# Optimization experiments

Hardware: AMD Instinct MI355X
Metric: run time of the kernel (lower is better)

## Reference

```python
import jax, jax.numpy as jnp
import numpy as np

B, H, E_DIM, V = 512, 2048, 1024, 50257


def setup_inputs() -> dict:
    key = jax.random.key(0)
    ks = jax.random.split(key, 10)
    s_e = 1.0 / np.sqrt(E_DIM)
    s_h = 1.0 / np.sqrt(H)
    return {
        "inp": jax.random.randint(ks[0], (B,), 0, V),
        "h_0": jax.random.normal(ks[1], (B, H), jnp.float32) * 0.1,
        "c_0": jax.random.normal(ks[2], (B, H), jnp.float32) * 0.1,
        "E": jax.random.normal(ks[3], (V, E_DIM), jnp.float32),
        "Wx": jax.random.normal(ks[4], (4, H, E_DIM), jnp.float32) * s_e,
        "bx": jax.random.normal(ks[5], (4, H), jnp.float32) * s_e,
        "Wh": jax.random.normal(ks[6], (4, H, H), jnp.float32) * s_h,
        "bh": jax.random.normal(ks[7], (4, H), jnp.float32) * s_h,
        "Wd": jax.random.normal(ks[8], (V, H), jnp.float32) * s_h,
        "bd": jax.random.normal(ks[9], (V,), jnp.float32) * s_h,
    }


def reference(inp, h_0, c_0, E, Wx, bx, Wh, bh, Wd, bd):
    # Embedding lookup: [B, E_DIM]
    x = E[inp]
    # Two fused GEMMs for all 4 gates (gate order: f, i, o, c): [B, 4, H]
    gates = (jnp.einsum('be,ghe->bgh', x, Wx) + bx[None]
             + jnp.einsum('bh,gkh->bgk', h_0, Wh) + bh[None])
    f_g = jax.nn.sigmoid(gates[:, 0])
    i_g = jax.nn.sigmoid(gates[:, 1])
    o_g = jax.nn.sigmoid(gates[:, 2])
    c_tilda = jnp.tanh(gates[:, 3])
    cx = f_g * c_0 + i_g * c_tilda
    hx = o_g * jnp.tanh(cx)
    out = hx @ Wd.T + bd  # [B, V]
    return out, hx, cx
```

## Files before the change

kernel.cpp:

```cpp
#include <hip/hip_runtime.h>
#include <hip/hip_bf16.h>

using bf16x8 = __attribute__((ext_vector_type(8))) short;
using f32x4  = __attribute__((ext_vector_type(4))) float;

#define DEVI __device__ __forceinline__

DEVI unsigned short bf16r(float f)
{
    return __builtin_bit_cast(unsigned short, __float2bfloat16(f));
}

DEVI bf16x8 cvt8(const f32x4 a, const f32x4 b)
{
    bf16x8 r;
#pragma unroll
    for (int j = 0; j < 4; ++j) {
        r[j]     = (short)bf16r(a[j]);
        r[4 + j] = (short)bf16r(b[j]);
    }
    return r;
}

__global__ __launch_bounds__(256) void k_gather(const float* __restrict__ E,
                                                const int* __restrict__ inp,
                                                unsigned short* __restrict__ x)
{
    const int b = blockIdx.x;
    const long r = inp[b];
    const f32x4 v = ((const f32x4*)(E + r * 1024L))[threadIdx.x];
    ushort4 o;
    o.x = bf16r(v[0]); o.y = bf16r(v[1]); o.z = bf16r(v[2]); o.w = bf16r(v[3]);
    ((ushort4*)(x + (long)b * 1024L))[threadIdx.x] = o;
}

__global__ __launch_bounds__(256) void k_cvt(const float* __restrict__ in,
                                             unsigned short* __restrict__ out)
{
    const long i = (blockIdx.x * 256L + threadIdx.x) * 8;
    const f32x4 a = *(const f32x4*)(in + i);
    const f32x4 b = *(const f32x4*)(in + i + 4);
    *(bf16x8*)(out + i) = cvt8(a, b);
}


DEVI bf16x8 lds_frag(const char* lds, int row, int j)
{
    return *(const bf16x8*)(lds + row * 128 + ((j ^ (row & 7)) << 4));
}

DEVI void mfma_tile(const char* sA, const char* sB, int l, int wr, int wc,
                    f32x4 (&acc)[4][4])
{
#pragma unroll
    for (int ks = 0; ks < 2; ++ks) {
        bf16x8 af[4], bq[4];
#pragma unroll
        for (int m = 0; m < 4; ++m)
            af[m] = lds_frag(sA, wr * 64 + m * 16 + (l & 15), ks * 4 + (l >> 4));
#pragma unroll
        for (int n = 0; n < 4; ++n)
            bq[n] = lds_frag(sB, wc * 64 + n * 16 + (l & 15), ks * 4 + (l >> 4));
#pragma unroll
        for (int m = 0; m < 4; ++m)
#pragma unroll
            for (int n = 0; n < 4; ++n)
                acc[m][n] = __builtin_amdgcn_mfma_f32_16x16x32_bf16(
                    af[m], bq[n], acc[m][n], 0, 0, 0);
    }
}

template <bool CLAMP>
DEVI void gemm_core(const unsigned short* __restrict__ A, long lda, long arow0,
                    const float* __restrict__ B, long ldb, long brow0, long bmax,
                    int ntiles, long kbase, int t,
                    char* sA0, char* sB0, char* sA1, char* sB1,
                    f32x4 (&acc)[4][4])
{
    const int l = t & 63;
    const int wr = (t >> 7) & 1, wc = (t >> 6) & 1;

    const unsigned short* ap[4];
#pragma unroll
    for (int i = 0; i < 4; ++i) {
        const int g = i * 256 + t, row = g >> 3, js = g & 7;
        ap[i] = A + (arow0 + row) * lda + kbase + (long)((js ^ (row & 7)) * 8);
    }
    const float* bp[4];
    int swz[4];
#pragma unroll
    for (int i = 0; i < 4; ++i) {
        const int g = i * 256 + t, row = g >> 3, j = g & 7;
        long br = brow0 + row;
        if (CLAMP) br = (br < bmax) ? br : (bmax - 1);
        bp[i] = B + br * ldb + kbase + (long)(j * 8);
        swz[i] = row * 128 + ((j ^ (row & 7)) << 4);
    }

    f32x4 b0lo[4], b0hi[4], b1lo[4], b1hi[4];

#define LOADB(lo, hi)                                                          \
    do {                                                                       \
        _Pragma("unroll") for (int i = 0; i < 4; ++i) {                        \
            lo[i] = *(const f32x4*)bp[i];                                      \
            hi[i] = *(const f32x4*)(bp[i] + 4);                                \
            bp[i] += 64;                                                       \
        }                                                                      \
    } while (0)
#define DMA_A(buf)                                                             \
    do {                                                                       \
        _Pragma("unroll") for (int i = 0; i < 4; ++i) {                        \
            __builtin_amdgcn_global_load_lds(                                  \
                (const __attribute__((address_space(1))) void*)(ap[i]),        \
                (__attribute__((address_space(3))) void*)((buf) +              \
                                                          (i * 256 + t) * 16), \
                16, 0, 0);                                                     \
            ap[i] += 64;                                                       \
        }                                                                      \
    } while (0)
#define WRITEB(buf, lo, hi)                                                    \
    do {                                                                       \
        _Pragma("unroll") for (int i = 0; i < 4; ++i)                          \
            *(bf16x8*)((buf) + swz[i]) = cvt8(lo[i], hi[i]);                   \
    } while (0)

    LOADB(b0lo, b0hi);
    DMA_A(sA0);
    WRITEB(sB0, b0lo, b0hi);
    LOADB(b1lo, b1hi);
    __syncthreads();

    for (int ti = 0; ti < ntiles; ti += 2) {
        DMA_A(sA1);
        if (ti + 2 < ntiles) LOADB(b0lo, b0hi);
        WRITEB(sB1, b1lo, b1hi);
        mfma_tile(sA0, sB0, l, wr, wc, acc);
        __syncthreads();
        if (ti + 2 < ntiles) {
            DMA_A(sA0);
            if (ti + 3 < ntiles) LOADB(b1lo, b1hi);
            WRITEB(sB0, b0lo, b0hi);
        }
        mfma_tile(sA1, sB1, l, wr, wc, acc);
        __syncthreads();
    }
#undef LOADB
#undef DMA_A
#undef WRITEB
}

__global__ __launch_bounds__(256, 2) void k_gates(
    const unsigned short* __restrict__ xb, const float* __restrict__ Wx,
    const unsigned short* __restrict__ h0b, const float* __restrict__ Wh,
    float* __restrict__ g0, float* __restrict__ g1, float* __restrict__ g2)
{
    __shared__ __align__(16) char sA0[128 * 128], sB0[128 * 128];
    __shared__ __align__(16) char sA1[128 * 128], sB1[128 * 128];
    const int t = threadIdx.x;
    const int bid = blockIdx.x;
    const int xcd = bid & 7, slot = bid >> 3;
    const int L = xcd * 96 + slot;
    const int mtile = L & 3;
    const int rest = L >> 2;
    const int ntile = rest & 63;
    const int z = rest >> 6;

    const unsigned short* A; const float* B; long lda, ldb, kbase; float* C;
    if (z == 0)      { A = xb;  lda = 1024; B = Wx; ldb = 1024; kbase = 0;    C = g0; }
    else if (z == 1) { A = h0b; lda = 2048; B = Wh; ldb = 2048; kbase = 0;    C = g1; }
    else             { A = h0b; lda = 2048; B = Wh; ldb = 2048; kbase = 1024; C = g2; }

    f32x4 acc[4][4] = {};
    gemm_core<false>(A, lda, (long)mtile * 128, B, ldb, (long)ntile * 128,
                     1L << 40, 16, kbase, t, sA0, sB0, sA1, sB1, acc);

    const int l = t & 63;
    const int wr = (t >> 7) & 1, wc = (t >> 6) & 1;
    const int lc = l & 15, r4 = (l >> 4) * 4;
#pragma unroll
    for (int n = 0; n < 4; ++n) {
        const long col = (long)ntile * 128 + wc * 64 + n * 16 + lc;
#pragma unroll
        for (int m = 0; m < 4; ++m) {
            const long row = (long)mtile * 128 + wr * 64 + m * 16 + r4;
#pragma unroll
            for (int r = 0; r < 4; ++r)
                C[(row + r) * 8192 + col] = acc[m][n][r];
        }
    }
}

__global__ __launch_bounds__(256, 2) void k_dec(
    const unsigned short* __restrict__ hxb, const float* __restrict__ Wd,
    const float* __restrict__ bd, float* __restrict__ out)
{
    __shared__ __align__(16) char sA0[128 * 128], sB0[128 * 128];
    __shared__ __align__(16) char sA1[128 * 128], sB1[128 * 128];
    const int t = threadIdx.x;
    const int bid = blockIdx.x;
    const int xcd = bid & 7, slot = bid >> 3;
    const int L = xcd * 196 + (xcd < 4 ? xcd : 4) + slot;
    const int mtile = L & 3;
    const int ntile = L >> 2;
    const long N = 50257;

    f32x4 acc[4][4] = {};
    gemm_core<true>(hxb, 2048, (long)mtile * 128, Wd, 2048, (long)ntile * 128,
                    N, 32, 0, t, sA0, sB0, sA1, sB1, acc);

    const int l = t & 63;
    const int wr = (t >> 7) & 1, wc = (t >> 6) & 1;
    const int lc = l & 15, r4 = (l >> 4) * 4;
#pragma unroll
    for (int n = 0; n < 4; ++n) {
        const long col = (long)ntile * 128 + wc * 64 + n * 16 + lc;
        if (col >= N) continue;
        const float bias = bd[col];
#pragma unroll
        for (int m = 0; m < 4; ++m) {
            const long row = (long)mtile * 128 + wr * 64 + m * 16 + r4;
#pragma unroll
            for (int r = 0; r < 4; ++r)
                out[(row + r) * N + col] = acc[m][n][r] + bias;
        }
    }
}

__global__ __launch_bounds__(256) void k_lstm(
    const float* __restrict__ g0, const float* __restrict__ g1,
    const float* __restrict__ g2, const float* __restrict__ bx,
    const float* __restrict__ bh, const float* __restrict__ c0,
    float* __restrict__ hx, float* __restrict__ cx,
    unsigned short* __restrict__ hxb)
{
    const int i = blockIdx.x * 256 + threadIdx.x;
    const int b = i >> 9;
    const int hc = (i & 511) << 2;
    const long base = (long)b * 8192;

    f32x4 g[4];
#pragma unroll
    for (int gi = 0; gi < 4; ++gi) {
        const long off = base + gi * 2048 + hc;
        const int boff = gi * 2048 + hc;
        g[gi] = *(const f32x4*)(g0 + off);
        g[gi] += *(const f32x4*)(g1 + off);
        g[gi] += *(const f32x4*)(g2 + off);
        g[gi] += *(const f32x4*)(bx + boff);
        g[gi] += *(const f32x4*)(bh + boff);
    }
    const f32x4 c0v = *(const f32x4*)(c0 + (long)b * 2048 + hc);

    f32x4 cv, hv;
    ushort4 hb;
#pragma unroll
    for (int j = 0; j < 4; ++j) {
        const float fg = 1.f / (1.f + __expf(-g[0][j]));
        const float ig = 1.f / (1.f + __expf(-g[1][j]));
        const float og = 1.f / (1.f + __expf(-g[2][j]));
        const float e2 = __expf(2.f * g[3][j]);
        const float ct = 1.f - 2.f / (e2 + 1.f);
        const float c  = fg * c0v[j] + ig * ct;
        const float e2c = __expf(2.f * c);
        const float th  = 1.f - 2.f / (e2c + 1.f);
        cv[j] = c;
        hv[j] = og * th;
    }
    hb.x = bf16r(hv[0]); hb.y = bf16r(hv[1]); hb.z = bf16r(hv[2]); hb.w = bf16r(hv[3]);

    const long o = (long)b * 2048 + hc;
    *(f32x4*)(cx + o) = cv;
    *(f32x4*)(hx + o) = hv;
    *(ushort4*)(hxb + o) = hb;
}

extern "C" void kernel_launch(void* const* d_in, const int* in_sizes, int n_in,
                              void* d_out, int out_size, void* d_ws, size_t ws_size,
                              hipStream_t stream)
{
    const int*   inp = (const int*)d_in[0];
    const float* h0  = (const float*)d_in[1];
    const float* c0  = (const float*)d_in[2];
    const float* E   = (const float*)d_in[3];
    const float* Wx  = (const float*)d_in[4];
    const float* bx  = (const float*)d_in[5];
    const float* Wh  = (const float*)d_in[6];
    const float* bh  = (const float*)d_in[7];
    const float* Wd  = (const float*)d_in[8];
    const float* bd  = (const float*)d_in[9];

    float* out = (float*)d_out;
    float* hx  = out + 512L * 50257L;
    float* cx  = hx + 512L * 2048L;

    unsigned short* xb  = (unsigned short*)out;
    float* g0 = out + (1L << 20);
    float* g1 = out + (5L << 20);
    float* g2 = out + (9L << 20);
    unsigned short* h0b = (unsigned short*)(out + (13L << 20));
    unsigned short* hxb = (unsigned short*)d_ws;

    k_gather<<<512, 256, 0, stream>>>(E, inp, xb);
    k_cvt<<<512, 256, 0, stream>>>(h0, h0b);

    k_gates<<<768, 256, 0, stream>>>(xb, Wx, h0b, Wh, g0, g1, g2);

    k_lstm<<<1024, 256, 0, stream>>>(g0, g1, g2, bx, bh, c0, hx, cx, hxb);

    k_dec<<<1572, 256, 0, stream>>>(hxb, Wd, bd, out);
}
```

Measured before the change: 285.6 us.

## Triple-buffer A tiles and replace syncthreads with fine-grained vmcnt waits

The GEMM core pipeline is restructured to use three LDS buffers for the DMA'd A tiles and two for B, with explicit s_waitcnt vmcnt/lgkmcnt and raw s_barrier in place of __syncthreads. This lets the next A tile's global-to-LDS load be issued before the current tile's MFMAs without a full drain of outstanding memory ops, aiming to overlap loads with compute more deeply. LDS use per block rises from 64KB to 80KB, which may reduce occupancy at two blocks per CU. The hand-tuned vmcnt counts depend on the exact number of outstanding loads and are fragile if the load pattern changes.

```diff
diff --git a/kernel.cpp b/kernel.cpp
--- a/kernel.cpp
+++ b/kernel.cpp
@@ -74,7 +74,7 @@
 DEVI void gemm_core(const unsigned short* __restrict__ A, long lda, long arow0,
                     const float* __restrict__ B, long ldb, long brow0, long bmax,
                     int ntiles, long kbase, int t,
-                    char* sA0, char* sB0, char* sA1, char* sB1,
+                    char* sA , char* sB ,
                     f32x4 (&acc)[4][4])
 {
     const int l = t & 63;
@@ -107,46 +107,64 @@
             bp[i] += 64;                                                       \
         }                                                                      \
     } while (0)
-#define DMA_A(buf)                                                             \
+#define DMA_A(bufidx)                                                          \
     do {                                                                       \
+        char* _d = sA + (bufidx) * 16384;                                      \
         _Pragma("unroll") for (int i = 0; i < 4; ++i) {                        \
             __builtin_amdgcn_global_load_lds(                                  \
                 (const __attribute__((address_space(1))) void*)(ap[i]),        \
-                (__attribute__((address_space(3))) void*)((buf) +              \
+                (__attribute__((address_space(3))) void*)(_d +                 \
                                                           (i * 256 + t) * 16), \
                 16, 0, 0);                                                     \
             ap[i] += 64;                                                       \
         }                                                                      \
     } while (0)
-#define WRITEB(buf, lo, hi)                                                    \
+#define WRITEB(bufofs, lo, hi)                                                 \
     do {                                                                       \
         _Pragma("unroll") for (int i = 0; i < 4; ++i)                          \
-            *(bf16x8*)((buf) + swz[i]) = cvt8(lo[i], hi[i]);                   \
+            *(bf16x8*)(sB + (bufofs) + swz[i]) = cvt8(lo[i], hi[i]);           \
     } while (0)
+#define WAITV12 asm volatile("s_waitcnt vmcnt(12)" ::: "memory")
+#define WAITV0  asm volatile("s_waitcnt vmcnt(0)" ::: "memory")
+#define WAITL0  asm volatile("s_waitcnt lgkmcnt(0)" ::: "memory")
+#define BARRIER __builtin_amdgcn_s_barrier()
 
     LOADB(b0lo, b0hi);
-    DMA_A(sA0);
-    WRITEB(sB0, b0lo, b0hi);
+    DMA_A(0);
+
+    int abuf = 0;
+    for (int ti = 0; ti < ntiles - 2; ti += 2) {
+        LOADB(b1lo, b1hi);
+        DMA_A((abuf + 1) % 3);
+        WAITV12;
+        WRITEB(0, b0lo, b0hi);
+        WAITL0; BARRIER;
+        mfma_tile(sA + abuf * 16384, sB, l, wr, wc, acc);
+        LOADB(b0lo, b0hi);
+        DMA_A((abuf + 2) % 3);
+        WAITV12;
+        WRITEB(16384, b1lo, b1hi);
+        WAITL0; BARRIER;
+        mfma_tile(sA + ((abuf + 1) % 3) * 16384, sB + 16384, l, wr, wc, acc);
+        abuf = (abuf + 2) % 3;
+    }
     LOADB(b1lo, b1hi);
-    __syncthreads();
-
-    for (int ti = 0; ti < ntiles; ti += 2) {
-        DMA_A(sA1);
-        if (ti + 2 < ntiles) LOADB(b0lo, b0hi);
-        WRITEB(sB1, b1lo, b1hi);
-        mfma_tile(sA0, sB0, l, wr, wc, acc);
-        __syncthreads();
-        if (ti + 2 < ntiles) {
-            DMA_A(sA0);
-            if (ti + 3 < ntiles) LOADB(b1lo, b1hi);
-            WRITEB(sB0, b0lo, b0hi);
-        }
-        mfma_tile(sA1, sB1, l, wr, wc, acc);
-        __syncthreads();
-    }
+    DMA_A((abuf + 1) % 3);
+    WAITV12;
+    WRITEB(0, b0lo, b0hi);
+    WAITL0; BARRIER;
+    mfma_tile(sA + abuf * 16384, sB, l, wr, wc, acc);
+    WAITV0;
+    WRITEB(16384, b1lo, b1hi);
+    WAITL0; BARRIER;
+    mfma_tile(sA + ((abuf + 1) % 3) * 16384, sB + 16384, l, wr, wc, acc);
 #undef LOADB
 #undef DMA_A
 #undef WRITEB
+#undef WAITV12
+#undef WAITV0
+#undef WAITL0
+#undef BARRIER
 }
 
 __global__ __launch_bounds__(256, 2) void k_gates(
@@ -154,8 +172,8 @@
     const unsigned short* __restrict__ h0b, const float* __restrict__ Wh,
     float* __restrict__ g0, float* __restrict__ g1, float* __restrict__ g2)
 {
-    __shared__ __align__(16) char sA0[128 * 128], sB0[128 * 128];
-    __shared__ __align__(16) char sA1[128 * 128], sB1[128 * 128];
+    __shared__ __align__(16) char sA[3 * 16384];
+    __shared__ __align__(16) char sB[2 * 16384];
     const int t = threadIdx.x;
     const int bid = blockIdx.x;
     const int xcd = bid & 7, slot = bid >> 3;
@@ -172,7 +190,7 @@
 
     f32x4 acc[4][4] = {};
     gemm_core<false>(A, lda, (long)mtile * 128, B, ldb, (long)ntile * 128,
-                     1L << 40, 16, kbase, t, sA0, sB0, sA1, sB1, acc);
+                     1L << 40, 16, kbase, t, sA, sB, acc);
 
     const int l = t & 63;
     const int wr = (t >> 7) & 1, wc = (t >> 6) & 1;
@@ -194,8 +212,8 @@
     const unsigned short* __restrict__ hxb, const float* __restrict__ Wd,
     const float* __restrict__ bd, float* __restrict__ out)
 {
-    __shared__ __align__(16) char sA0[128 * 128], sB0[128 * 128];
-    __shared__ __align__(16) char sA1[128 * 128], sB1[128 * 128];
+    __shared__ __align__(16) char sA[3 * 16384];
+    __shared__ __align__(16) char sB[2 * 16384];
     const int t = threadIdx.x;
     const int bid = blockIdx.x;
     const int xcd = bid & 7, slot = bid >> 3;
@@ -206,7 +224,7 @@
 
     f32x4 acc[4][4] = {};
     gemm_core<true>(hxb, 2048, (long)mtile * 128, Wd, 2048, (long)ntile * 128,
-                    N, 32, 0, t, sA0, sB0, sA1, sB1, acc);
+                    N, 32, 0, t, sA, sB, acc);
 
     const int l = t & 63;
     const int wr = (t >> 7) & 1, wc = (t >> 6) & 1;
```

New measurement: 305.1 us. 6.8% more time.

## Use 256x128 tiles with 8 waves and register-staged A loads

Applied to the files above, without the earlier changes.

Grows the GEMM block tile from 128x128 to 256x128 and runs 8 waves (512 threads) per block, so each fp32 weight tile converted to bf16 is reused across twice as many batch rows. Weight traffic and conversion work for the large decoder GEMM should roughly halve. A is now loaded through registers and written to LDS instead of the direct global-to-LDS path, with hand-placed vmcnt/lgkmcnt waits and raw barriers. The kernels also need 96KB of dynamic LDS, which may limit how many blocks fit per CU, and the manual waitcnt scheduling is fragile.

```diff
diff --git a/kernel.cpp b/kernel.cpp
--- a/kernel.cpp
+++ b/kernel.cpp
@@ -34,8 +34,8 @@
     ((ushort4*)(x + (long)b * 1024L))[threadIdx.x] = o;
 }
 
-__global__ __launch_bounds__(256) void k_cvt(const float* __restrict__ in,
-                                             unsigned short* __restrict__ out)
+__global__ __launch_bounds__(256) void k_cvtn(const float* __restrict__ in,
+                                              unsigned short* __restrict__ out)
 {
     const long i = (blockIdx.x * 256L + threadIdx.x) * 8;
     const f32x4 a = *(const f32x4*)(in + i);
@@ -49,8 +49,8 @@
     return *(const bf16x8*)(lds + row * 128 + ((j ^ (row & 7)) << 4));
 }
 
-DEVI void mfma_tile(const char* sA, const char* sB, int l, int wr, int wc,
-                    f32x4 (&acc)[4][4])
+DEVI void mfma_tile8(const char* sA, const char* sB, int l, int wr, int wc,
+                     f32x4 (&acc)[4][4])
 {
 #pragma unroll
     for (int ks = 0; ks < 2; ++ks) {
@@ -71,118 +71,122 @@
 }
 
 template <bool CLAMP>
-DEVI void gemm_core(const unsigned short* __restrict__ A, long lda, long arow0,
-                    const float* __restrict__ B, long ldb, long brow0, long bmax,
-                    int ntiles, long kbase, int t,
-                    char* sA0, char* sB0, char* sA1, char* sB1,
-                    f32x4 (&acc)[4][4])
-{
-    const int l = t & 63;
-    const int wr = (t >> 7) & 1, wc = (t >> 6) & 1;
+DEVI void gemm_core8(const unsigned short* __restrict__ A, long lda, long arow0,
+                     const float* __restrict__ B, long ldb, long brow0, long bmax,
+                     int nt, long kbase, int t, char* lds, f32x4 (&acc)[4][4])
+{
+    char* sA0 = lds;
+    char* sA1 = lds + 32768;
+    char* sB0 = lds + 65536;
+    char* sB1 = lds + 81920;
+    const int l = t & 63, w = t >> 6, wr = w >> 1, wc = w & 1;
 
     const unsigned short* ap[4];
+    int aswz[4];
 #pragma unroll
     for (int i = 0; i < 4; ++i) {
-        const int g = i * 256 + t, row = g >> 3, js = g & 7;
-        ap[i] = A + (arow0 + row) * lda + kbase + (long)((js ^ (row & 7)) * 8);
-    }
-    const float* bp[4];
-    int swz[4];
-#pragma unroll
-    for (int i = 0; i < 4; ++i) {
-        const int g = i * 256 + t, row = g >> 3, j = g & 7;
+        const int g = i * 512 + t, row = g >> 3, j = g & 7;
+        ap[i] = A + (arow0 + row) * lda + kbase + j * 8;
+        aswz[i] = row * 128 + ((j ^ (row & 7)) << 4);
+    }
+    const float* bp[2];
+    int bswz[2];
+#pragma unroll
+    for (int i = 0; i < 2; ++i) {
+        const int g = i * 512 + t, row = g >> 3, j = g & 7;
         long br = brow0 + row;
         if (CLAMP) br = (br < bmax) ? br : (bmax - 1);
-        bp[i] = B + br * ldb + kbase + (long)(j * 8);
-        swz[i] = row * 128 + ((j ^ (row & 7)) << 4);
-    }
-
-    f32x4 b0lo[4], b0hi[4], b1lo[4], b1hi[4];
-
-#define LOADB(lo, hi)                                                          \
+        bp[i] = B + br * ldb + kbase + j * 8;
+        bswz[i] = row * 128 + ((j ^ (row & 7)) << 4);
+    }
+
+    bf16x8 ra0[4], ra1[4];
+    f32x4 rb0[4], rb1[4];
+
+#define LOADR(as, bs)                                                          \
     do {                                                                       \
         _Pragma("unroll") for (int i = 0; i < 4; ++i) {                        \
-            lo[i] = *(const f32x4*)bp[i];                                      \
-            hi[i] = *(const f32x4*)(bp[i] + 4);                                \
+            as[i] = *(const bf16x8*)ap[i];                                     \
+            ap[i] += 64;                                                       \
+        }                                                                      \
+        _Pragma("unroll") for (int i = 0; i < 2; ++i) {                        \
+            bs[2 * i]     = *(const f32x4*)bp[i];                              \
+            bs[2 * i + 1] = *(const f32x4*)(bp[i] + 4);                        \
             bp[i] += 64;                                                       \
         }                                                                      \
     } while (0)
-#define DMA_A(buf)                                                             \
-    do {                                                                       \
-        _Pragma("unroll") for (int i = 0; i < 4; ++i) {                        \
-            __builtin_amdgcn_global_load_lds(                                  \
-                (const __attribute__((address_space(1))) void*)(ap[i]),        \
-                (__attribute__((address_space(3))) void*)((buf) +              \
-                                                          (i * 256 + t) * 16), \
-                16, 0, 0);                                                     \
-            ap[i] += 64;                                                       \
-        }                                                                      \
-    } while (0)
-#define WRITEB(buf, lo, hi)                                                    \
+#define WRLDS(sa, sb, as, bs)                                                  \
     do {                                                                       \
         _Pragma("unroll") for (int i = 0; i < 4; ++i)                          \
-            *(bf16x8*)((buf) + swz[i]) = cvt8(lo[i], hi[i]);                   \
+            *(bf16x8*)((sa) + aswz[i]) = as[i];                                \
+        _Pragma("unroll") for (int i = 0; i < 2; ++i)                          \
+            *(bf16x8*)((sb) + bswz[i]) = cvt8(bs[2 * i], bs[2 * i + 1]);       \
     } while (0)
-
-    LOADB(b0lo, b0hi);
-    DMA_A(sA0);
-    WRITEB(sB0, b0lo, b0hi);
-    LOADB(b1lo, b1hi);
-    __syncthreads();
-
-    for (int ti = 0; ti < ntiles; ti += 2) {
-        DMA_A(sA1);
-        if (ti + 2 < ntiles) LOADB(b0lo, b0hi);
-        WRITEB(sB1, b1lo, b1hi);
-        mfma_tile(sA0, sB0, l, wr, wc, acc);
-        __syncthreads();
-        if (ti + 2 < ntiles) {
-            DMA_A(sA0);
-            if (ti + 3 < ntiles) LOADB(b1lo, b1hi);
-            WRITEB(sB0, b0lo, b0hi);
+#define WAITV8  asm volatile("s_waitcnt vmcnt(8)" ::: "memory")
+#define WAITV0  asm volatile("s_waitcnt vmcnt(0)" ::: "memory")
+#define WAITL0  asm volatile("s_waitcnt lgkmcnt(0)" ::: "memory")
+#define BARRIER __builtin_amdgcn_s_barrier()
+
+    LOADR(ra0, rb0);
+    LOADR(ra1, rb1);
+    WAITV8;
+    WRLDS(sA0, sB0, ra0, rb0);
+    LOADR(ra0, rb0);
+    WAITL0; BARRIER;
+
+    for (int kt = 0; kt < nt; kt += 2) {
+        if (kt + 2 < nt) WAITV8; else WAITV0;
+        WRLDS(sA1, sB1, ra1, rb1);
+        if (kt + 3 < nt) LOADR(ra1, rb1);
+        mfma_tile8(sA0, sB0, l, wr, wc, acc);
+        WAITL0; BARRIER;
+        if (kt + 2 < nt) {
+            if (kt + 3 < nt) WAITV8; else WAITV0;
+            WRLDS(sA0, sB0, ra0, rb0);
+            if (kt + 4 < nt) LOADR(ra0, rb0);
         }
-        mfma_tile(sA1, sB1, l, wr, wc, acc);
-        __syncthreads();
-    }
-#undef LOADB
-#undef DMA_A
-#undef WRITEB
-}
-
-__global__ __launch_bounds__(256, 2) void k_gates(
+        mfma_tile8(sA1, sB1, l, wr, wc, acc);
+        WAITL0; BARRIER;
+    }
+#undef LOADR
+#undef WRLDS
+#undef WAITV8
+#undef WAITV0
+#undef WAITL0
+#undef BARRIER
+}
+
+__global__ __launch_bounds__(512, 2) void k_gates(
     const unsigned short* __restrict__ xb, const float* __restrict__ Wx,
     const unsigned short* __restrict__ h0b, const float* __restrict__ Wh,
     float* __restrict__ g0, float* __restrict__ g1, float* __restrict__ g2)
 {
-    __shared__ __align__(16) char sA0[128 * 128], sB0[128 * 128];
-    __shared__ __align__(16) char sA1[128 * 128], sB1[128 * 128];
+    extern __shared__ __align__(16) char lds[];
     const int t = threadIdx.x;
     const int bid = blockIdx.x;
     const int xcd = bid & 7, slot = bid >> 3;
-    const int L = xcd * 96 + slot;
-    const int mtile = L & 3;
-    const int rest = L >> 2;
-    const int ntile = rest & 63;
-    const int z = rest >> 6;
-
-    const unsigned short* A; const float* B; long lda, ldb, kbase; float* C;
-    if (z == 0)      { A = xb;  lda = 1024; B = Wx; ldb = 1024; kbase = 0;    C = g0; }
-    else if (z == 1) { A = h0b; lda = 2048; B = Wh; ldb = 2048; kbase = 0;    C = g1; }
-    else             { A = h0b; lda = 2048; B = Wh; ldb = 2048; kbase = 1024; C = g2; }
+    const int L = xcd * 48 + slot;
+    const int z = L >> 7;
+    const int mtile = L & 1;
+    const int ntile = (L >> 1) & 63;
+
+    const unsigned short* A; const float* B; long lda, ldb, kbase; float* C; int nt;
+    if (z == 0)      { A = xb;  lda = 1024; B = Wx; ldb = 1024; kbase = 0;    C = g0; nt = 16; }
+    else if (z == 1) { A = h0b; lda = 2048; B = Wh; ldb = 2048; kbase = 0;    C = g1; nt = 16; }
+    else             { A = h0b; lda = 2048; B = Wh; ldb = 2048; kbase = 1024; C = g2; nt = 16; }
 
     f32x4 acc[4][4] = {};
-    gemm_core<false>(A, lda, (long)mtile * 128, B, ldb, (long)ntile * 128,
-                     1L << 40, 16, kbase, t, sA0, sB0, sA1, sB1, acc);
-
-    const int l = t & 63;
-    const int wr = (t >> 7) & 1, wc = (t >> 6) & 1;
+    gemm_core8<false>(A, lda, (long)mtile * 256, B, ldb, (long)ntile * 128,
+                      1L << 40, nt, kbase, t, lds, acc);
+
+    const int l = t & 63, w = t >> 6, wr = w >> 1, wc = w & 1;
     const int lc = l & 15, r4 = (l >> 4) * 4;
 #pragma unroll
     for (int n = 0; n < 4; ++n) {
         const long col = (long)ntile * 128 + wc * 64 + n * 16 + lc;
 #pragma unroll
         for (int m = 0; m < 4; ++m) {
-            const long row = (long)mtile * 128 + wr * 64 + m * 16 + r4;
+            const long row = (long)mtile * 256 + wr * 64 + m * 16 + r4;
 #pragma unroll
             for (int r = 0; r < 4; ++r)
                 C[(row + r) * 8192 + col] = acc[m][n][r];
@@ -190,26 +194,24 @@
     }
 }
 
-__global__ __launch_bounds__(256, 2) void k_dec(
+__global__ __launch_bounds__(512, 2) void k_dec(
     const unsigned short* __restrict__ hxb, const float* __restrict__ Wd,
     const float* __restrict__ bd, float* __restrict__ out)
 {
-    __shared__ __align__(16) char sA0[128 * 128], sB0[128 * 128];
-    __shared__ __align__(16) char sA1[128 * 128], sB1[128 * 128];
+    extern __shared__ __align__(16) char lds[];
     const int t = threadIdx.x;
     const int bid = blockIdx.x;
     const int xcd = bid & 7, slot = bid >> 3;
-    const int L = xcd * 196 + (xcd < 4 ? xcd : 4) + slot;
-    const int mtile = L & 3;
-    const int ntile = L >> 2;
+    const int L = (xcd < 2) ? (xcd * 99 + slot) : (198 + (xcd - 2) * 98 + slot);
+    const int mtile = L & 1;
+    const int ntile = L >> 1;
     const long N = 50257;
 
     f32x4 acc[4][4] = {};
-    gemm_core<true>(hxb, 2048, (long)mtile * 128, Wd, 2048, (long)ntile * 128,
-                    N, 32, 0, t, sA0, sB0, sA1, sB1, acc);
-
-    const int l = t & 63;
-    const int wr = (t >> 7) & 1, wc = (t >> 6) & 1;
+    gemm_core8<true>(hxb, 2048, (long)mtile * 256, Wd, 2048, (long)ntile * 128,
+                     N, 32, 0, t, lds, acc);
+
+    const int l = t & 63, w = t >> 6, wr = w >> 1, wc = w & 1;
     const int lc = l & 15, r4 = (l >> 4) * 4;
 #pragma unroll
     for (int n = 0; n < 4; ++n) {
@@ -218,7 +220,7 @@
         const float bias = bd[col];
 #pragma unroll
         for (int m = 0; m < 4; ++m) {
-            const long row = (long)mtile * 128 + wr * 64 + m * 16 + r4;
+            const long row = (long)mtile * 256 + wr * 64 + m * 16 + r4;
 #pragma unroll
             for (int r = 0; r < 4; ++r)
                 out[(row + r) * N + col] = acc[m][n][r] + bias;
@@ -301,11 +303,11 @@
     unsigned short* hxb = (unsigned short*)d_ws;
 
     k_gather<<<512, 256, 0, stream>>>(E, inp, xb);
-    k_cvt<<<512, 256, 0, stream>>>(h0, h0b);
-
-    k_gates<<<768, 256, 0, stream>>>(xb, Wx, h0b, Wh, g0, g1, g2);
+    k_cvtn<<<512, 256, 0, stream>>>(h0, h0b);
+
+    k_gates<<<384, 512, 98304, stream>>>(xb, Wx, h0b, Wh, g0, g1, g2);
 
     k_lstm<<<1024, 256, 0, stream>>>(g0, g1, g2, bx, bh, c0, hx, cx, hxb);
 
-    k_dec<<<1572, 256, 0, stream>>>(hxb, Wd, bd, out);
-}
+    k_dec<<<786, 512, 98304, stream>>>(hxb, Wd, bd, out);
+}
```

Result: no change. 284.8 us (-0.3%).
